# Performance work log

Measured on AMD Instinct MI355X. Metric: run time of the kernel, lower is better.

The kernel has to match this reference:

```python
import jax, jax.numpy as jnp
import numpy as np

BS, NQ, NC = 128, 900, 91
PRE_TOPK = 10000      # source: pre_topk when n_queries*n_cls > 10000
POST_TOPK = 100       # source: keep_inds[:100]
IOU_THRESH = 0.7


def box_cxcywh_to_xyxy(b):
    cx, cy, w, h = b[..., 0], b[..., 1], b[..., 2], b[..., 3]
    return jnp.stack([cx - 0.5 * w, cy - 0.5 * h, cx + 0.5 * w, cy + 0.5 * h], axis=-1)


def nms_image(boxes, scores, labels):
    """Greedy batched NMS, returning the first POST_TOPK picked indices.
    boxes: [PRE,4] xyxy (scaled), scores: [PRE] desc-sorted, labels: [PRE] int.
    batched_nms trick: offset boxes per class so IoU across classes is 0."""
    max_coord = jnp.max(boxes)
    off = labels.astype(boxes.dtype) * (max_coord + 1.0)
    ob = boxes + off[:, None]                          # [PRE,4]
    areas = (ob[:, 2] - ob[:, 0]) * (ob[:, 3] - ob[:, 1])

    def step(active, _):
        s = jnp.where(active, scores, -jnp.inf)
        i = jnp.argmax(s)                              # highest-score surviving box
        bi = ob[i]
        xx1 = jnp.maximum(bi[0], ob[:, 0])
        yy1 = jnp.maximum(bi[1], ob[:, 1])
        xx2 = jnp.minimum(bi[2], ob[:, 2])
        yy2 = jnp.minimum(bi[3], ob[:, 3])
        inter = jnp.clip(xx2 - xx1, 0.0) * jnp.clip(yy2 - yy1, 0.0)
        union = areas[i] + areas - inter
        iou = inter / jnp.maximum(union, 1e-9)
        # suppress IoU > thresh (includes i itself since iou(i,i)=1)
        active = active & (iou <= IOU_THRESH)
        return active, i

    _, keep = jax.lax.scan(step, jnp.ones(ob.shape[0], dtype=bool), None, length=POST_TOPK)
    return keep                                         # [POST]


def setup_inputs() -> dict:
    key = jax.random.key(0)
    k1, k2, k3, k4 = jax.random.split(key, 4)
    pred_logits = jax.random.normal(k1, (BS, NQ, NC), dtype=jnp.float32) * 2.0 - 2.0
    cxcy = jax.random.uniform(k2, (BS, NQ, 2), dtype=jnp.float32)
    wh = jax.random.uniform(k3, (BS, NQ, 2), dtype=jnp.float32, minval=0.02, maxval=0.3)
    pred_boxes = jnp.concatenate([cxcy, wh], axis=-1)   # cxcywh in [0,1]
    target_sizes = jax.random.uniform(k4, (BS, 2), dtype=jnp.float32, minval=480.0, maxval=1333.0)
    return {"pred_logits": pred_logits, "pred_boxes": pred_boxes, "target_sizes": target_sizes}


def reference(pred_logits, pred_boxes, target_sizes):
    bs, nq, nc = pred_logits.shape
    prob = jax.nn.sigmoid(pred_logits).reshape(bs, nq * nc)      # all_scores
    boxes = box_cxcywh_to_xyxy(pred_boxes)                        # [bs,nq,4]
    img_h, img_w = target_sizes[:, 0], target_sizes[:, 1]
    scale = jnp.stack([img_w, img_h, img_w, img_h], axis=1)       # [bs,4]
    boxes = boxes * scale[:, None, :]

    top_scores, top_idx = jax.lax.top_k(prob, PRE_TOPK)           # [bs,PRE]
    top_labels = top_idx % nc                                     # all_labels gather
    top_box_idx = top_idx // nc                                   # all_boxes gather
    top_boxes = jnp.take_along_axis(boxes, top_box_idx[..., None], axis=1)  # [bs,PRE,4]

    keep = jax.vmap(nms_image)(top_boxes, top_scores, top_labels)  # [bs,POST]
    out_scores = jnp.take_along_axis(top_scores, keep, axis=1)
    out_labels = jnp.take_along_axis(top_labels, keep, axis=1)
    out_boxes = jnp.take_along_axis(top_boxes, keep[..., None], axis=1)
    return out_scores, out_labels, out_boxes
```

## Files before the change

### kernel.cpp

```cpp
#include <hip/hip_runtime.h>
#include <cstdint>

#pragma clang fp contract(off)

#define BS   128
#define NQ   900
#define NC   91
#define NQC  (NQ * NC)
#define Q4   (NQC / 4)
#define HHALF 10238
#define PRE  10000
#define POST 100
#define TBITS 13
#define TBINS (1 << TBITS)
#define TSHIFT (32 - TBITS)
#define K_WIN 16
#define HSEG 1024
#define KS   2780
#define CAPH 7680
#define NSLOT 15

typedef unsigned long long ull;

#define WS_CNT 0
#define WS_KEYS 8192

__device__ __forceinline__ uint32_t fkey(float f) {
    uint32_t b = __float_as_uint(f);
    return (b & 0x80000000u) ? ~b : (b | 0x80000000u);
}
__device__ __forceinline__ float unkey(uint32_t u) {
    uint32_t b = (u & 0x80000000u) ? (u & 0x7FFFFFFFu) : ~u;
    return __uint_as_float(b);
}
__device__ __forceinline__ uint32_t qclamp(uint32_t q) { return (q < NQ) ? q : (NQ - 1); }

__device__ __forceinline__ ull shflx(ull v, int j) {
    uint32_t lo = (uint32_t)__shfl_xor((int)(uint32_t)v, j, 64);
    uint32_t hi = (uint32_t)__shfl_xor((int)(uint32_t)(v >> 32), j, 64);
    return ((ull)hi << 32) | (ull)lo;
}
__device__ __forceinline__ ull cex(ull v, int j, bool lower, bool desc) {
    ull pb = shflx(v, j);
    ull a = lower ? v : pb;
    ull b = lower ? pb : v;
    bool sw = desc ? (a < b) : (a > b);
    return sw ? pb : v;
}
__device__ __forceinline__ void ce(ull& a, ull& b, bool desc) {
    bool sw = desc ? (a < b) : (a > b);
    if (sw) { ull t = a; a = b; b = t; }
}

__global__ void __launch_bounds__(1024) k_compact(const float* __restrict__ logits,
                                                  ull* __restrict__ keys,
                                                  uint32_t* __restrict__ cnts) {
    const int img = blockIdx.x >> 1;
    const int h = blockIdx.x & 1;
    const int tid = threadIdx.x;
    const int lane = tid & 63;
    __shared__ uint32_t hist[TBINS];
    __shared__ uint32_t part[1024];
    __shared__ uint32_t sTB, sCnt;
    const float4* lg4 = (const float4*)(logits + (size_t)img * NQC);
    for (int i = tid; i < TBINS; i += 1024) hist[i] = 0u;
    if (tid == 0) sCnt = 0u;
    float4 sv[5];
    #pragma unroll
    for (int c = 0; c < 5; ++c) sv[c] = lg4[c * 4096 + tid];
    __syncthreads();
    #pragma unroll
    for (int c = 0; c < 5; ++c) {
        atomicAdd(&hist[fkey(sv[c].x) >> TSHIFT], 1u);
        atomicAdd(&hist[fkey(sv[c].y) >> TSHIFT], 1u);
        atomicAdd(&hist[fkey(sv[c].z) >> TSHIFT], 1u);
        atomicAdd(&hist[fkey(sv[c].w) >> TSHIFT], 1u);
    }
    __syncthreads();
    {
        uint32_t s = 0;
        int b0 = tid * 8;
        #pragma unroll
        for (int j = 0; j < 8; ++j) s += hist[b0 + j];
        part[tid] = s;
    }
    __syncthreads();
    if (tid < 64) {
        uint32_t pv[16]; uint32_t tot = 0;
        #pragma unroll
        for (int j = 0; j < 16; ++j) { pv[j] = part[tid * 16 + j]; tot += pv[j]; }
        uint32_t sinc = tot;
        #pragma unroll
        for (int off = 1; off < 64; off <<= 1) {
            uint32_t o = (uint32_t)__shfl_down((int)sinc, off, 64);
            if (tid + off < 64) sinc += o;
        }
        uint32_t cum = sinc - tot;
        for (int j = 15; j >= 0; --j) {
            if (cum < KS && cum + pv[j] >= KS) {
                int pbn = (tid * 16 + j) * 8;
                uint32_t c2 = cum;
                for (int b = pbn + 7; b >= pbn; --b) {
                    if (c2 + hist[b] >= KS) { sTB = (uint32_t)b; break; }
                    c2 += hist[b];
                }
            }
            cum += pv[j];
        }
    }
    __syncthreads();
    const uint32_t TB = sTB;
    ull* seg = keys + (size_t)(img * 2 + h) * CAPH;
    const int lo = h * HHALF;
    const int hi = (lo + HHALF < Q4) ? (lo + HHALF) : Q4;
    for (int i0 = lo; i0 < hi; i0 += 1024) {
        int i = i0 + tid;
        bool inb = (i < hi);
        float4 v = inb ? lg4[i] : make_float4(0.f, 0.f, 0.f, 0.f);
        float comp[4] = {v.x, v.y, v.z, v.w};
        #pragma unroll
        for (int c = 0; c < 4; ++c) {
            uint32_t u = fkey(comp[c]);
            bool pass = inb && ((u >> TSHIFT) >= TB);
            ull m = __ballot(pass);
            if (m) {
                uint32_t wb = 0u;
                if (lane == 0) wb = atomicAdd(&sCnt, (uint32_t)__popcll(m));
                wb = (uint32_t)__shfl((int)wb, 0, 64);
                if (pass) {
                    uint32_t p = wb + (uint32_t)__popcll(m & ((1ull << lane) - 1ull));
                    uint32_t fi = (uint32_t)(i * 4 + c);
                    if (p < CAPH) seg[p] = ((ull)u << 32) | (ull)(0xFFFFFFFFu - fi);
                }
            }
        }
    }
    __syncthreads();
    if (tid == 0) cnts[img * 2 + h] = (sCnt < CAPH) ? sCnt : CAPH;
}

__global__ void __launch_bounds__(1024) k_sel(const ull* __restrict__ keys,
                                              const uint32_t* __restrict__ cnts,
                                              const float* __restrict__ pred_boxes,
                                              const float* __restrict__ target_sizes,
                                              float* __restrict__ out) {
    const int img = blockIdx.x;
    const int tid = threadIdx.x;
    const int lane = tid & 63;
    const int wv = tid >> 6;

    __shared__ uint32_t hist[TBINS];
    __shared__ uint32_t part[1024];
    __shared__ float4 shPB[NQ];
    __shared__ ull binK[HSEG];
    __shared__ ull headK[HSEG];
    __shared__ float aX1[POST], aY1[POST], aX2[POST], aY2[POST], aAr[POST];
    __shared__ int   aCl[POST];
    __shared__ float s_x1[K_WIN], s_y1[K_WIN], s_x2[K_WIN], s_y2[K_WIN];
    __shared__ int   s_cl[K_WIN];
    __shared__ uint32_t s_em[K_WIN];
    __shared__ ull sF0;
    __shared__ uint32_t sCntA, sCntB, sMX;
    __shared__ uint32_t sB1, sTp1, sB2, sTp2, sTK;

    const float ih = target_sizes[img * 2 + 0];
    const float iw = target_sizes[img * 2 + 1];
    const float* pb = pred_boxes + (size_t)img * NQ * 4;

    auto mckey = [&](uint32_t f) -> uint32_t {
        uint32_t q = qclamp(f / NC);
        float4 bb = shPB[q];
        float x1 = (bb.x - 0.5f * bb.z) * iw;
        float y1 = (bb.y - 0.5f * bb.w) * ih;
        float x2 = (bb.x + 0.5f * bb.z) * iw;
        float y2 = (bb.y + 0.5f * bb.w) * ih;
        return fkey(fmaxf(fmaxf(x1, y1), fmaxf(x2, y2)));
    };

    if (tid < NQ) shPB[tid] = ((const float4*)pb)[tid];
    for (int i = tid; i < TBINS; i += 1024) hist[i] = 0u;
    binK[tid] = 0ull; headK[tid] = 0ull;
    if (tid == 0) { sCntA = 0u; sCntB = 0u; sMX = 0u; sF0 = 0ull;
                    sB1 = 0u; sTp1 = 1u; sB2 = 0u; sTp2 = 0u; sTK = 0u; }
    const uint32_t c0 = cnts[img * 2 + 0];
    const uint32_t c1 = cnts[img * 2 + 1];
    const int total = (int)(c0 + c1);
    const ull* seg0 = keys + (size_t)(img * 2) * CAPH;
    const ull* seg1 = seg0 + CAPH;
    ull kk[NSLOT];
    #pragma unroll
    for (int j = 0; j < NSLOT; ++j) {
        int i = tid + (j << 10);
        ull x = 0ull;
        if (i < total) x = (i < (int)c0) ? seg0[i] : seg1[i - (int)c0];
        kk[j] = x;
    }
    __syncthreads();

    #pragma unroll
    for (int j = 0; j < NSLOT; ++j) {
        ull x = kk[j];
        if (x != 0ull) atomicAdd(&hist[(uint32_t)(x >> 51)], 1u);
    }
    __syncthreads();
    {
        uint32_t s = 0;
        int b0 = tid * 8;
        #pragma unroll
        for (int j = 0; j < 8; ++j) s += hist[b0 + j];
        part[tid] = s;
    }
    __syncthreads();
    if (tid < 64) {
        uint32_t pv[16]; uint32_t tot = 0;
        #pragma unroll
        for (int j = 0; j < 16; ++j) { pv[j] = part[tid * 16 + j]; tot += pv[j]; }
        uint32_t sinc = tot;
        #pragma unroll
        for (int off = 1; off < 64; off <<= 1) {
            uint32_t o = (uint32_t)__shfl_down((int)sinc, off, 64);
            if (tid + off < 64) sinc += o;
        }
        uint32_t tt = (uint32_t)__shfl((int)sinc, 0, 64);
        uint32_t TKl = (tt < PRE) ? tt : PRE;
        uint32_t T2l = (TKl < HSEG) ? TKl : HSEG;
        if (tid == 0) sTK = TKl;
        uint32_t cum = sinc - tot;
        for (int j = 15; j >= 0; --j) {
            if (cum < TKl && cum + pv[j] >= TKl) {
                int pbn = (tid * 16 + j) * 8;
                uint32_t c2 = cum;
                for (int b = pbn + 7; b >= pbn; --b) {
                    if (c2 + hist[b] >= TKl) { sB1 = (uint32_t)b; sTp1 = TKl - c2; break; }
                    c2 += hist[b];
                }
            }
            if (cum < T2l && cum + pv[j] >= T2l) {
                int pbn = (tid * 16 + j) * 8;
                uint32_t c2 = cum;
                for (int b = pbn + 7; b >= pbn; --b) {
                    if (c2 + hist[b] >= T2l) { sB2 = (uint32_t)b; sTp2 = T2l - c2; break; }
                    c2 += hist[b];
                }
            }
            cum += pv[j];
        }
    }
    __syncthreads();
    const uint32_t B1 = sB1, tp1 = sTp1, B2 = sB2;
    const uint32_t TK = sTK;
    const int C1 = (int)(((TK < (uint32_t)HSEG) ? TK : (uint32_t)HSEG) - sTp2);

    uint32_t lmx = 0u;
    #pragma unroll
    for (int j = 0; j < NSLOT; ++j) {
        ull x = kk[j];
        uint32_t bin = (uint32_t)(x >> 51);
        bool liveK = (x != 0ull);
        if (liveK && bin > B1) { uint32_t km = mckey(~(uint32_t)x); if (km > lmx) lmx = km; }
        bool isA = liveK && (bin == B1);
        bool isB = liveK && (bin > B2);
        ull mA = __ballot(isA);
        if (mA) {
            uint32_t wb = 0u;
            if (lane == 0) wb = atomicAdd(&sCntA, (uint32_t)__popcll(mA));
            wb = (uint32_t)__shfl((int)wb, 0, 64);
            if (isA) {
                uint32_t p = wb + (uint32_t)__popcll(mA & ((1ull << lane) - 1ull));
                if (p < HSEG) binK[p] = x;
            }
        }
        ull mB = __ballot(isB);
        if (mB) {
            uint32_t wb = 0u;
            if (lane == 0) wb = atomicAdd(&sCntB, (uint32_t)__popcll(mB));
            wb = (uint32_t)__shfl((int)wb, 0, 64);
            if (isB) {
                uint32_t p = wb + (uint32_t)__popcll(mB & ((1ull << lane) - 1ull));
                if (p < HSEG) headK[p] = x;
            }
        }
    }
    __syncthreads();

    {
        ull r0 = 0, r1 = 0, r2 = 0, r3 = 0;
        const int cw = wv & 3;
        const int cb = cw << 8;
        ull* A = (wv < 4) ? binK : headK;
        if (wv < 8) {
            r0 = A[cb | lane]; r1 = A[cb | 64 | lane];
            r2 = A[cb | 128 | lane]; r3 = A[cb | 192 | lane];
            #pragma unroll
            for (int k2 = 2; k2 <= 32; k2 <<= 1) {
                bool d = ((lane & k2) == 0);
                #pragma unroll
                for (int j = 16; j >= 1; j >>= 1) {
                    if (j <= (k2 >> 1)) {
                        bool lw = ((lane & j) == 0);
                        r0 = cex(r0, j, lw, d); r1 = cex(r1, j, lw, d);
                        r2 = cex(r2, j, lw, d); r3 = cex(r3, j, lw, d);
                    }
                }
            }
            #pragma unroll
            for (int j = 32; j >= 1; j >>= 1) {
                bool lw = ((lane & j) == 0);
                r0 = cex(r0, j, lw, true);  r1 = cex(r1, j, lw, false);
                r2 = cex(r2, j, lw, true);  r3 = cex(r3, j, lw, false);
            }
            ce(r0, r1, true); ce(r2, r3, false);
            #pragma unroll
            for (int j = 32; j >= 1; j >>= 1) {
                bool lw = ((lane & j) == 0);
                r0 = cex(r0, j, lw, true);  r1 = cex(r1, j, lw, true);
                r2 = cex(r2, j, lw, false); r3 = cex(r3, j, lw, false);
            }
            {
                bool d = ((cw & 1) == 0);
                ce(r0, r2, d); ce(r1, r3, d); ce(r0, r1, d); ce(r2, r3, d);
                #pragma unroll
                for (int j = 32; j >= 1; j >>= 1) {
                    bool lw = ((lane & j) == 0);
                    r0 = cex(r0, j, lw, d); r1 = cex(r1, j, lw, d);
                    r2 = cex(r2, j, lw, d); r3 = cex(r3, j, lw, d);
                }
            }
            A[cb | lane] = r0; A[cb | 64 | lane] = r1;
            A[cb | 128 | lane] = r2; A[cb | 192 | lane] = r3;
        }
        __syncthreads();
        {
            ull* Bp = (tid >> 9) ? headK : binK;
            int t = tid & 511;
            int i = ((t & ~255) << 1) | (t & 255);
            int ixj = i | 256;
            bool d = ((i & 512) == 0);
            ull a = Bp[i], b = Bp[ixj];
            bool sw = d ? (a < b) : (a > b);
            if (sw) { Bp[i] = b; Bp[ixj] = a; }
        }
        __syncthreads();
        if (wv < 8) {
            r0 = A[cb | lane]; r1 = A[cb | 64 | lane];
            r2 = A[cb | 128 | lane]; r3 = A[cb | 192 | lane];
            bool d = ((cw & 2) == 0);
            ce(r0, r2, d); ce(r1, r3, d); ce(r0, r1, d); ce(r2, r3, d);
            #pragma unroll
            for (int j = 32; j >= 1; j >>= 1) {
                bool lw = ((lane & j) == 0);
                r0 = cex(r0, j, lw, d); r1 = cex(r1, j, lw, d);
                r2 = cex(r2, j, lw, d); r3 = cex(r3, j, lw, d);
            }
            A[cb | lane] = r0; A[cb | 64 | lane] = r1;
            A[cb | 128 | lane] = r2; A[cb | 192 | lane] = r3;
        }
        __syncthreads();
        {
            ull* Bp = (tid >> 9) ? headK : binK;
            int t = tid & 511;
            ull a = Bp[t], b = Bp[t | 512];
            if (a < b) { Bp[t] = b; Bp[t | 512] = a; }
        }
        __syncthreads();
        {
            ull* Bp = (tid >> 9) ? headK : binK;
            int t = tid & 511;
            int i = ((t & ~255) << 1) | (t & 255);
            int ixj = i | 256;
            ull a = Bp[i], b = Bp[ixj];
            if (a < b) { Bp[i] = b; Bp[ixj] = a; }
        }
        __syncthreads();
        if (wv < 8) {
            r0 = A[cb | lane]; r1 = A[cb | 64 | lane];
            r2 = A[cb | 128 | lane]; r3 = A[cb | 192 | lane];
            ce(r0, r2, true); ce(r1, r3, true); ce(r0, r1, true); ce(r2, r3, true);
            #pragma unroll
            for (int j = 32; j >= 1; j >>= 1) {
                bool lw = ((lane & j) == 0);
                r0 = cex(r0, j, lw, true); r1 = cex(r1, j, lw, true);
                r2 = cex(r2, j, lw, true); r3 = cex(r3, j, lw, true);
            }
            A[cb | lane] = r0; A[cb | 64 | lane] = r1;
            A[cb | 128 | lane] = r2; A[cb | 192 | lane] = r3;
        }
        __syncthreads();
    }

    if (tid < (int)tp1) {
        ull x = binK[tid];
        if (x != 0ull) { uint32_t km = mckey(~(uint32_t)x); if (km > lmx) lmx = km; }
    }
    for (int off = 32; off > 0; off >>= 1) {
        uint32_t o = (uint32_t)__shfl_down((int)lmx, off, 64);
        if (o > lmx) lmx = o;
    }
    if (lane == 0) atomicMax(&sMX, lmx);
    if (tid == 0 && C1 > 0) sF0 = headK[0];
    __syncthreads();
    float offD;
    {
        uint32_t m = sMX;
        uint32_t b = (m & 0x80000000u) ? (m & 0x7FFFFFFFu) : ~m;
        offD = __uint_as_float(b) + 1.0f;
    }

    auto sort1024 = [&]() {
        const int idx = tid;
        ull x = headK[idx];
        #pragma unroll
        for (int k2 = 2; k2 <= 32; k2 <<= 1) {
            bool d = ((lane & k2) == 0);
            #pragma unroll
            for (int j = 16; j >= 1; j >>= 1)
                if (j <= (k2 >> 1)) x = cex(x, j, (lane & j) == 0, d);
        }
        {
            bool d = ((idx & 64) == 0);
            #pragma unroll
            for (int j = 32; j >= 1; j >>= 1) x = cex(x, j, (lane & j) == 0, d);
        }
        for (int k = 128; k <= 1024; k <<= 1) {
            headK[idx] = x;
            __syncthreads();
            for (int j = k >> 1; j >= 64; j >>= 1) {
                if (tid < 512) {
                    int i2 = ((tid & ~(j - 1)) << 1) | (tid & (j - 1));
                    int ixj = i2 | j;
                    ull a = headK[i2], b = headK[ixj];
                    bool sw = ((i2 & k) == 0) ? (a < b) : (a > b);
                    if (sw) { headK[i2] = b; headK[ixj] = a; }
                }
                __syncthreads();
            }
            x = headK[idx];
            bool d = ((idx & k) == 0);
            #pragma unroll
            for (int j = 32; j >= 1; j >>= 1) x = cex(x, j, (lane & j) == 0, d);
        }
        headK[idx] = x;
        __syncthreads();
    };

    int npick = 0, base = 0, segbase = 0, segend = C1;
    int bcur = (int)B2;
    bool needF0 = (C1 == 0);
    while (npick < POST) {
        if (base >= segend) {
            if (segend >= (int)TK) {
                ull x0 = sF0;
                uint32_t f0 = ~(uint32_t)x0;
                uint32_t u0 = (uint32_t)(x0 >> 32);
                uint32_t q0 = qclamp(f0 / NC);
                uint32_t cc0 = f0 - (f0 / NC) * NC;
                float4 bb = shPB[q0];
                float rx1 = (bb.x - 0.5f * bb.z) * iw;
                float ry1 = (bb.y - 0.5f * bb.w) * ih;
                float rx2 = (bb.x + 0.5f * bb.z) * iw;
                float ry2 = (bb.y + 0.5f * bb.w) * ih;
                float sc = 1.0f / (1.0f + expf(-unkey(u0)));
                for (int p2 = npick + tid; p2 < POST; p2 += 1024) {
                    out[img * POST + p2] = sc;
                    out[BS * POST + img * POST + p2] = (float)cc0;
                    float* ob2 = out + 2 * BS * POST + ((size_t)img * POST + p2) * 4;
                    ob2[0] = rx1; ob2[1] = ry1; ob2[2] = rx2; ob2[3] = ry2;
                }
                break;
            }
            while (bcur > 0 && hist[bcur] == 0u) --bcur;
            headK[tid] = 0ull;
            if (tid == 0) sCntA = 0u;
            __syncthreads();
            for (int i0 = 0; i0 < total; i0 += 1024) {
                int i = i0 + tid;
                ull x = 0ull;
                if (i < total) x = (i < (int)c0) ? seg0[i] : seg1[i - (int)c0];
                bool pass = (x != 0ull) && ((uint32_t)(x >> 51) == (uint32_t)bcur);
                ull m = __ballot(pass);
                if (m) {
                    uint32_t wb = 0u;
                    if (lane == 0) wb = atomicAdd(&sCntA, (uint32_t)__popcll(m));
                    wb = (uint32_t)__shfl((int)wb, 0, 64);
                    if (pass) {
                        uint32_t p = wb + (uint32_t)__popcll(m & ((1ull << lane) - 1ull));
                        if (p < HSEG) headK[p] = x;
                    }
                }
            }
            __syncthreads();
            sort1024();
            int avail = (int)((sCntA < (uint32_t)HSEG) ? sCntA : (uint32_t)HSEG);
            int take = (int)TK - segend; if (take > avail) take = avail;
            if (needF0) { if (tid == 0) sF0 = headK[0]; needF0 = false; __syncthreads(); }
            segbase = segend; segend += take; --bcur;
            continue;
        }

        const int r = base + wv;
        const bool val = (r < segend);
        const ull xk = headK[val ? (r - segbase) : 0];
        const uint32_t f = val ? ~(uint32_t)xk : 0u;
        const uint32_t uk = (uint32_t)(xk >> 32);
        const uint32_t q = qclamp(f / NC);
        const uint32_t cc = f - (f / NC) * NC;
        float4 bb = shPB[q];
        const float x1 = (bb.x - 0.5f * bb.z) * iw;
        const float y1 = (bb.y - 0.5f * bb.w) * ih;
        const float x2 = (bb.x + 0.5f * bb.z) * iw;
        const float y2 = (bb.y + 0.5f * bb.w) * ih;
        if (lane == 0) {
            s_x1[wv] = x1; s_y1[wv] = y1; s_x2[wv] = x2; s_y2[wv] = y2;
            s_cl[wv] = val ? (int)cc : -1;
        }
        __syncthreads();

        const float o = (float)cc * offD;
        const float cx1 = x1 + o, cy1 = y1 + o, cx2 = x2 + o, cy2 = y2 + o;
        const float car = (cx2 - cx1) * (cy2 - cy1);
        bool cf = false;
        if (val && lane < wv && s_cl[lane] == (int)cc) {
            float jx1 = s_x1[lane] + o, jy1 = s_y1[lane] + o;
            float jx2 = s_x2[lane] + o, jy2 = s_y2[lane] + o;
            float arj = (jx2 - jx1) * (jy2 - jy1);
            float xx1 = fmaxf(jx1, cx1), yy1 = fmaxf(jy1, cy1);
            float xx2 = fminf(jx2, cx2), yy2 = fminf(jy2, cy2);
            float inter = fmaxf(xx2 - xx1, 0.0f) * fmaxf(yy2 - yy1, 0.0f);
            float uni = (arj + car) - inter;
            float iou = inter / fmaxf(uni, 1e-9f);
            cf = !(iou <= 0.7f);
        }
        uint32_t em = (uint32_t)(__ballot(cf) & 0xFFFFull);
        bool pf = false;
        for (int i2 = lane; i2 < npick; i2 += 64) {
            if (aCl[i2] == (int)cc) {
                float jx1 = aX1[i2] + o, jy1 = aY1[i2] + o;
                float jx2 = aX2[i2] + o, jy2 = aY2[i2] + o;
                float arj = aAr[i2];
                float xx1 = fmaxf(jx1, cx1), yy1 = fmaxf(jy1, cy1);
                float xx2 = fminf(jx2, cx2), yy2 = fminf(jy2, cy2);
                float inter = fmaxf(xx2 - xx1, 0.0f) * fmaxf(yy2 - yy1, 0.0f);
                float uni = (arj + car) - inter;
                float iou = inter / fmaxf(uni, 1e-9f);
                pf |= !(iou <= 0.7f);
            }
        }
        bool anyPrior = (__ballot(pf) != 0ull);
        if (lane == 0)
            s_em[wv] = em | (anyPrior ? 0x80000000u : 0u) | (val ? 0u : 0x40000000u);
        __syncthreads();

        uint32_t acc = 0u; int a = 0;
        const int room = POST - npick;
        #pragma unroll
        for (int w2 = 0; w2 < K_WIN; ++w2) {
            uint32_t ew = s_em[w2];
            if (!(ew & 0xC0000000u) && a < room && ((ew & 0xFFFFu & acc) == 0u)) {
                acc |= (1u << w2); ++a;
            }
        }

        if (((acc >> wv) & 1u) && lane == 0) {
            int p = npick + __popc(acc & ((1u << wv) - 1u));
            float sc = 1.0f / (1.0f + expf(-unkey(uk)));
            out[img * POST + p] = sc;
            out[BS * POST + img * POST + p] = (float)cc;
            float* ob2 = out + 2 * BS * POST + ((size_t)img * POST + p) * 4;
            ob2[0] = x1; ob2[1] = y1; ob2[2] = x2; ob2[3] = y2;
            aX1[p] = x1; aY1[p] = y1; aX2[p] = x2; aY2[p] = y2;
            aAr[p] = car; aCl[p] = (int)cc;
        }
        npick += a;
        base += K_WIN;
    }
}

extern "C" void kernel_launch(void* const* d_in, const int* in_sizes, int n_in,
                              void* d_out, int out_size, void* d_ws, size_t ws_size,
                              hipStream_t stream) {
    const float* logits = (const float*)d_in[0];
    const float* boxes  = (const float*)d_in[1];
    const float* tsizes = (const float*)d_in[2];
    float* out = (float*)d_out;

    uint32_t* cnts = (uint32_t*)((char*)d_ws + WS_CNT);
    ull* keys = (ull*)((char*)d_ws + WS_KEYS);

    k_compact<<<2 * BS, 1024, 0, stream>>>(logits, keys, cnts);
    k_sel<<<BS, 1024, 0, stream>>>(keys, cnts, boxes, tsizes, out);
}
```

Baseline: 138.8 us.

## Precompute selection histograms in compact kernel and widen NMS window to 64

The compact kernel now builds a histogram of the candidate keys it writes and stores it to global memory as uint16 per half-image. The select kernel sums the two half histograms instead of re-histogramming every candidate with shared atomics. The greedy NMS window grows from 16 to 64 candidates per round, with each wave handling four candidates, so there are fewer block-wide synchronisations. In exchange, each round does more speculative IoU work that may be wasted, and the kernels use more registers and extra workspace.

Measured after the change: 146.9 us. 1.06x slower.

```diff
diff --git a/kernel.cpp b/kernel.cpp
--- a/kernel.cpp
+++ b/kernel.cpp
@@ -14,7 +14,7 @@
 #define TBITS 13
 #define TBINS (1 << TBITS)
 #define TSHIFT (32 - TBITS)
-#define K_WIN 16
+#define K_WIN 64
 #define HSEG 1024
 #define KS   2780
 #define CAPH 7680
@@ -23,7 +23,8 @@
 typedef unsigned long long ull;
 
 #define WS_CNT 0
-#define WS_KEYS 8192
+#define WS_GH  4096
+#define WS_KEYS (4096 + 4*1024*1024)
 
 __device__ __forceinline__ uint32_t fkey(float f) {
     uint32_t b = __float_as_uint(f);
@@ -54,6 +55,7 @@
 
 __global__ void __launch_bounds__(1024) k_compact(const float* __restrict__ logits,
                                                   ull* __restrict__ keys,
+                                                  uint16_t* __restrict__ ghist,
                                                   uint32_t* __restrict__ cnts) {
     const int img = blockIdx.x >> 1;
     const int h = blockIdx.x & 1;
@@ -110,6 +112,8 @@
     }
     __syncthreads();
     const uint32_t TB = sTB;
+    for (int i = tid; i < TBINS; i += 1024) hist[i] = 0u;
+    __syncthreads();
     ull* seg = keys + (size_t)(img * 2 + h) * CAPH;
     const int lo = h * HHALF;
     const int hi = (lo + HHALF < Q4) ? (lo + HHALF) : Q4;
@@ -130,16 +134,22 @@
                 if (pass) {
                     uint32_t p = wb + (uint32_t)__popcll(m & ((1ull << lane) - 1ull));
                     uint32_t fi = (uint32_t)(i * 4 + c);
-                    if (p < CAPH) seg[p] = ((ull)u << 32) | (ull)(0xFFFFFFFFu - fi);
-                }
-            }
-        }
-    }
-    __syncthreads();
+                    if (p < CAPH) {
+                        seg[p] = ((ull)u << 32) | (ull)(0xFFFFFFFFu - fi);
+                        atomicAdd(&hist[u >> TSHIFT], 1u);
+                    }
+                }
+            }
+        }
+    }
+    __syncthreads();
+    uint16_t* g = ghist + (size_t)(img * 2 + h) * TBINS;
+    for (int i = tid; i < TBINS; i += 1024) g[i] = (uint16_t)hist[i];
     if (tid == 0) cnts[img * 2 + h] = (sCnt < CAPH) ? sCnt : CAPH;
 }
 
 __global__ void __launch_bounds__(1024) k_sel(const ull* __restrict__ keys,
+                                              const uint16_t* __restrict__ ghist,
                                               const uint32_t* __restrict__ cnts,
                                               const float* __restrict__ pred_boxes,
                                               const float* __restrict__ target_sizes,
@@ -158,7 +168,7 @@
     __shared__ int   aCl[POST];
     __shared__ float s_x1[K_WIN], s_y1[K_WIN], s_x2[K_WIN], s_y2[K_WIN];
     __shared__ int   s_cl[K_WIN];
-    __shared__ uint32_t s_em[K_WIN];
+    __shared__ ull   s_em[K_WIN];
     __shared__ ull sF0;
     __shared__ uint32_t sCntA, sCntB, sMX;
     __shared__ uint32_t sB1, sTp1, sB2, sTp2, sTK;
@@ -178,10 +188,22 @@
     };
 
     if (tid < NQ) shPB[tid] = ((const float4*)pb)[tid];
-    for (int i = tid; i < TBINS; i += 1024) hist[i] = 0u;
     binK[tid] = 0ull; headK[tid] = 0ull;
     if (tid == 0) { sCntA = 0u; sCntB = 0u; sMX = 0u; sF0 = 0ull;
                     sB1 = 0u; sTp1 = 1u; sB2 = 0u; sTp2 = 0u; sTK = 0u; }
+    {
+        const uint16_t* g0 = ghist + (size_t)(img * 2) * TBINS;
+        const uint16_t* g1 = g0 + TBINS;
+        uint32_t s = 0;
+        int b0 = tid * 8;
+        #pragma unroll
+        for (int j = 0; j < 8; ++j) {
+            uint32_t hv = (uint32_t)g0[b0 + j] + (uint32_t)g1[b0 + j];
+            hist[b0 + j] = hv;
+            s += hv;
+        }
+        part[tid] = s;
+    }
     const uint32_t c0 = cnts[img * 2 + 0];
     const uint32_t c1 = cnts[img * 2 + 1];
     const int total = (int)(c0 + c1);
@@ -197,20 +219,6 @@
     }
     __syncthreads();
 
-    #pragma unroll
-    for (int j = 0; j < NSLOT; ++j) {
-        ull x = kk[j];
-        if (x != 0ull) atomicAdd(&hist[(uint32_t)(x >> 51)], 1u);
-    }
-    __syncthreads();
-    {
-        uint32_t s = 0;
-        int b0 = tid * 8;
-        #pragma unroll
-        for (int j = 0; j < 8; ++j) s += hist[b0 + j];
-        part[tid] = s;
-    }
-    __syncthreads();
     if (tid < 64) {
         uint32_t pv[16]; uint32_t tot = 0;
         #pragma unroll
@@ -497,78 +505,111 @@
             continue;
         }
 
-        const int r = base + wv;
-        const bool val = (r < segend);
-        const ull xk = headK[val ? (r - segbase) : 0];
-        const uint32_t f = val ? ~(uint32_t)xk : 0u;
-        const uint32_t uk = (uint32_t)(xk >> 32);
-        const uint32_t q = qclamp(f / NC);
-        const uint32_t cc = f - (f / NC) * NC;
-        float4 bb = shPB[q];
-        const float x1 = (bb.x - 0.5f * bb.z) * iw;
-        const float y1 = (bb.y - 0.5f * bb.w) * ih;
-        const float x2 = (bb.x + 0.5f * bb.z) * iw;
-        const float y2 = (bb.y + 0.5f * bb.w) * ih;
+        bool valv[4]; uint32_t ccv[4], ukv[4];
+        float X1[4], Y1[4], X2[4], Y2[4];
+        #pragma unroll
+        for (int off = 0; off < 4; ++off) {
+            const int ci = 4 * wv + off;
+            const int r = base + ci;
+            valv[off] = (r < segend);
+            const ull xk = headK[valv[off] ? (r - segbase) : 0];
+            const uint32_t f = valv[off] ? ~(uint32_t)xk : 0u;
+            ukv[off] = (uint32_t)(xk >> 32);
+            const uint32_t q = qclamp(f / NC);
+            ccv[off] = f - (f / NC) * NC;
+            float4 bb = shPB[q];
+            X1[off] = (bb.x - 0.5f * bb.z) * iw;
+            Y1[off] = (bb.y - 0.5f * bb.w) * ih;
+            X2[off] = (bb.x + 0.5f * bb.z) * iw;
+            Y2[off] = (bb.y + 0.5f * bb.w) * ih;
+        }
         if (lane == 0) {
-            s_x1[wv] = x1; s_y1[wv] = y1; s_x2[wv] = x2; s_y2[wv] = y2;
-            s_cl[wv] = val ? (int)cc : -1;
-        }
-        __syncthreads();
-
-        const float o = (float)cc * offD;
-        const float cx1 = x1 + o, cy1 = y1 + o, cx2 = x2 + o, cy2 = y2 + o;
-        const float car = (cx2 - cx1) * (cy2 - cy1);
-        bool cf = false;
-        if (val && lane < wv && s_cl[lane] == (int)cc) {
-            float jx1 = s_x1[lane] + o, jy1 = s_y1[lane] + o;
-            float jx2 = s_x2[lane] + o, jy2 = s_y2[lane] + o;
-            float arj = (jx2 - jx1) * (jy2 - jy1);
-            float xx1 = fmaxf(jx1, cx1), yy1 = fmaxf(jy1, cy1);
-            float xx2 = fminf(jx2, cx2), yy2 = fminf(jy2, cy2);
-            float inter = fmaxf(xx2 - xx1, 0.0f) * fmaxf(yy2 - yy1, 0.0f);
-            float uni = (arj + car) - inter;
-            float iou = inter / fmaxf(uni, 1e-9f);
-            cf = !(iou <= 0.7f);
-        }
-        uint32_t em = (uint32_t)(__ballot(cf) & 0xFFFFull);
-        bool pf = false;
+            #pragma unroll
+            for (int off = 0; off < 4; ++off) {
+                const int ci = 4 * wv + off;
+                s_x1[ci] = X1[off]; s_y1[ci] = Y1[off];
+                s_x2[ci] = X2[off]; s_y2[ci] = Y2[off];
+                s_cl[ci] = valv[off] ? (int)ccv[off] : -1;
+            }
+        }
+        __syncthreads();
+
+        float ov[4], CX1[4], CY1[4], CX2[4], CY2[4], CAR[4];
+        ull emv[4];
+        #pragma unroll
+        for (int off = 0; off < 4; ++off) {
+            const int ci = 4 * wv + off;
+            const float o = (float)ccv[off] * offD;
+            ov[off] = o;
+            CX1[off] = X1[off] + o; CY1[off] = Y1[off] + o;
+            CX2[off] = X2[off] + o; CY2[off] = Y2[off] + o;
+            CAR[off] = (CX2[off] - CX1[off]) * (CY2[off] - CY1[off]);
+            bool cf = false;
+            if (valv[off] && lane < ci && s_cl[lane] == (int)ccv[off]) {
+                float jx1 = s_x1[lane] + o, jy1 = s_y1[lane] + o;
+                float jx2 = s_x2[lane] + o, jy2 = s_y2[lane] + o;
+                float arj = (jx2 - jx1) * (jy2 - jy1);
+                float xx1 = fmaxf(jx1, CX1[off]), yy1 = fmaxf(jy1, CY1[off]);
+                float xx2 = fminf(jx2, CX2[off]), yy2 = fminf(jy2, CY2[off]);
+                float inter = fmaxf(xx2 - xx1, 0.0f) * fmaxf(yy2 - yy1, 0.0f);
+                float uni = (arj + CAR[off]) - inter;
+                float iou = inter / fmaxf(uni, 1e-9f);
+                cf = !(iou <= 0.7f);
+            }
+            emv[off] = __ballot(cf) & ((ci == 0) ? 0ull : ((ci >= 64) ? ~0ull : ((1ull << ci) - 1ull)));
+        }
+        bool pf[4] = {false, false, false, false};
         for (int i2 = lane; i2 < npick; i2 += 64) {
-            if (aCl[i2] == (int)cc) {
-                float jx1 = aX1[i2] + o, jy1 = aY1[i2] + o;
-                float jx2 = aX2[i2] + o, jy2 = aY2[i2] + o;
-                float arj = aAr[i2];
-                float xx1 = fmaxf(jx1, cx1), yy1 = fmaxf(jy1, cy1);
-                float xx2 = fminf(jx2, cx2), yy2 = fminf(jy2, cy2);
-                float inter = fmaxf(xx2 - xx1, 0.0f) * fmaxf(yy2 - yy1, 0.0f);
-                float uni = (arj + car) - inter;
-                float iou = inter / fmaxf(uni, 1e-9f);
-                pf |= !(iou <= 0.7f);
-            }
-        }
-        bool anyPrior = (__ballot(pf) != 0ull);
-        if (lane == 0)
-            s_em[wv] = em | (anyPrior ? 0x80000000u : 0u) | (val ? 0u : 0x40000000u);
-        __syncthreads();
-
-        uint32_t acc = 0u; int a = 0;
+            const int acl = aCl[i2];
+            const float ax1 = aX1[i2], ay1 = aY1[i2], ax2 = aX2[i2], ay2 = aY2[i2];
+            const float aar = aAr[i2];
+            #pragma unroll
+            for (int off = 0; off < 4; ++off) {
+                if (valv[off] && acl == (int)ccv[off]) {
+                    float jx1 = ax1 + ov[off], jy1 = ay1 + ov[off];
+                    float jx2 = ax2 + ov[off], jy2 = ay2 + ov[off];
+                    float xx1 = fmaxf(jx1, CX1[off]), yy1 = fmaxf(jy1, CY1[off]);
+                    float xx2 = fminf(jx2, CX2[off]), yy2 = fminf(jy2, CY2[off]);
+                    float inter = fmaxf(xx2 - xx1, 0.0f) * fmaxf(yy2 - yy1, 0.0f);
+                    float uni = (aar + CAR[off]) - inter;
+                    float iou = inter / fmaxf(uni, 1e-9f);
+                    pf[off] |= !(iou <= 0.7f);
+                }
+            }
+        }
+        #pragma unroll
+        for (int off = 0; off < 4; ++off) {
+            bool anyP = (__ballot(pf[off]) != 0ull);
+            if (lane == 0) {
+                const int ci = 4 * wv + off;
+                s_em[ci] = emv[off] | ((anyP || !valv[off]) ? (1ull << 63) : 0ull);
+            }
+        }
+        __syncthreads();
+
+        ull acc = 0ull; int a = 0;
         const int room = POST - npick;
         #pragma unroll
-        for (int w2 = 0; w2 < K_WIN; ++w2) {
-            uint32_t ew = s_em[w2];
-            if (!(ew & 0xC0000000u) && a < room && ((ew & 0xFFFFu & acc) == 0u)) {
-                acc |= (1u << w2); ++a;
-            }
-        }
-
-        if (((acc >> wv) & 1u) && lane == 0) {
-            int p = npick + __popc(acc & ((1u << wv) - 1u));
-            float sc = 1.0f / (1.0f + expf(-unkey(uk)));
-            out[img * POST + p] = sc;
-            out[BS * POST + img * POST + p] = (float)cc;
-            float* ob2 = out + 2 * BS * POST + ((size_t)img * POST + p) * 4;
-            ob2[0] = x1; ob2[1] = y1; ob2[2] = x2; ob2[3] = y2;
-            aX1[p] = x1; aY1[p] = y1; aX2[p] = x2; aY2[p] = y2;
-            aAr[p] = car; aCl[p] = (int)cc;
+        for (int ci = 0; ci < K_WIN; ++ci) {
+            ull ew = s_em[ci];
+            if (!(ew >> 63) && a < room && ((ew & acc) == 0ull)) {
+                acc |= (1ull << ci); ++a;
+            }
+        }
+
+        #pragma unroll
+        for (int off = 0; off < 4; ++off) {
+            const int ci = 4 * wv + off;
+            if (((acc >> ci) & 1ull) && lane == off) {
+                int p = npick + (int)__popcll(acc & ((1ull << ci) - 1ull));
+                float sc = 1.0f / (1.0f + expf(-unkey(ukv[off])));
+                out[img * POST + p] = sc;
+                out[BS * POST + img * POST + p] = (float)ccv[off];
+                float* ob2 = out + 2 * BS * POST + ((size_t)img * POST + p) * 4;
+                ob2[0] = X1[off]; ob2[1] = Y1[off]; ob2[2] = X2[off]; ob2[3] = Y2[off];
+                aX1[p] = X1[off]; aY1[p] = Y1[off]; aX2[p] = X2[off]; aY2[p] = Y2[off];
+                aAr[p] = CAR[off]; aCl[p] = (int)ccv[off];
+            }
         }
         npick += a;
         base += K_WIN;
@@ -584,8 +625,9 @@
     float* out = (float*)d_out;
 
     uint32_t* cnts = (uint32_t*)((char*)d_ws + WS_CNT);
+    uint16_t* ghist = (uint16_t*)((char*)d_ws + WS_GH);
     ull* keys = (ull*)((char*)d_ws + WS_KEYS);
 
-    k_compact<<<2 * BS, 1024, 0, stream>>>(logits, keys, cnts);
-    k_sel<<<BS, 1024, 0, stream>>>(keys, cnts, boxes, tsizes, out);
-}
+    k_compact<<<2 * BS, 1024, 0, stream>>>(logits, keys, ghist, cnts);
+    k_sel<<<BS, 1024, 0, stream>>>(keys, ghist, cnts, boxes, tsizes, out);
+}
```

## Build selection histogram during compaction and batch per-wave atomics in compact loop

Applied to the files above, without the earlier changes.

The compaction kernel now builds a 13-bit histogram of the kept keys while writing them and stores it to workspace as uint16. The selection kernel reads both half-histograms instead of rebuilding one with shared atomics over all loaded keys, which removes a histogram pass and two barriers there. The compact loop also handles two float4 per thread per iteration and makes one atomic reservation per wave for all eight components instead of one per component. In exchange, compaction does extra shared atomics and global histogram writes, and the workspace layout grows.

Result: no change. 138.2 us (-0.4%).

```diff
diff --git a/kernel.cpp b/kernel.cpp
--- a/kernel.cpp
+++ b/kernel.cpp
@@ -23,7 +23,8 @@
 typedef unsigned long long ull;
 
 #define WS_CNT 0
-#define WS_KEYS 8192
+#define WS_GH  4096
+#define WS_KEYS (4096 + 4*1024*1024)
 
 __device__ __forceinline__ uint32_t fkey(float f) {
     uint32_t b = __float_as_uint(f);
@@ -54,6 +55,7 @@
 
 __global__ void __launch_bounds__(1024) k_compact(const float* __restrict__ logits,
                                                   ull* __restrict__ keys,
+                                                  uint16_t* __restrict__ ghist,
                                                   uint32_t* __restrict__ cnts) {
     const int img = blockIdx.x >> 1;
     const int h = blockIdx.x & 1;
@@ -110,36 +112,61 @@
     }
     __syncthreads();
     const uint32_t TB = sTB;
+    for (int i = tid; i < TBINS; i += 1024) hist[i] = 0u;
+    __syncthreads();
     ull* seg = keys + (size_t)(img * 2 + h) * CAPH;
     const int lo = h * HHALF;
     const int hi = (lo + HHALF < Q4) ? (lo + HHALF) : Q4;
-    for (int i0 = lo; i0 < hi; i0 += 1024) {
-        int i = i0 + tid;
-        bool inb = (i < hi);
-        float4 v = inb ? lg4[i] : make_float4(0.f, 0.f, 0.f, 0.f);
-        float comp[4] = {v.x, v.y, v.z, v.w};
-        #pragma unroll
-        for (int c = 0; c < 4; ++c) {
-            uint32_t u = fkey(comp[c]);
-            bool pass = inb && ((u >> TSHIFT) >= TB);
-            ull m = __ballot(pass);
-            if (m) {
-                uint32_t wb = 0u;
-                if (lane == 0) wb = atomicAdd(&sCnt, (uint32_t)__popcll(m));
-                wb = (uint32_t)__shfl((int)wb, 0, 64);
-                if (pass) {
-                    uint32_t p = wb + (uint32_t)__popcll(m & ((1ull << lane) - 1ull));
-                    uint32_t fi = (uint32_t)(i * 4 + c);
-                    if (p < CAPH) seg[p] = ((ull)u << 32) | (ull)(0xFFFFFFFFu - fi);
-                }
-            }
-        }
-    }
-    __syncthreads();
+    for (int i0 = lo; i0 < hi; i0 += 2048) {
+        float4 v[2]; bool inb[2]; int ii[2];
+        #pragma unroll
+        for (int s = 0; s < 2; ++s) {
+            int i = i0 + (s << 10) + tid;
+            ii[s] = i; inb[s] = (i < hi);
+            v[s] = inb[s] ? lg4[i] : make_float4(0.f, 0.f, 0.f, 0.f);
+        }
+        uint32_t u[8]; bool pass[8];
+        #pragma unroll
+        for (int s = 0; s < 2; ++s) {
+            u[s * 4 + 0] = fkey(v[s].x); u[s * 4 + 1] = fkey(v[s].y);
+            u[s * 4 + 2] = fkey(v[s].z); u[s * 4 + 3] = fkey(v[s].w);
+            #pragma unroll
+            for (int c = 0; c < 4; ++c)
+                pass[s * 4 + c] = inb[s] && ((u[s * 4 + c] >> TSHIFT) >= TB);
+        }
+        ull m[8]; uint32_t pc[8]; uint32_t tot = 0;
+        #pragma unroll
+        for (int c = 0; c < 8; ++c) {
+            m[c] = __ballot(pass[c]);
+            pc[c] = (uint32_t)__popcll(m[c]);
+            tot += pc[c];
+        }
+        uint32_t wb = 0u;
+        if (lane == 0 && tot) wb = atomicAdd(&sCnt, tot);
+        wb = (uint32_t)__shfl((int)wb, 0, 64);
+        ull lm = (1ull << lane) - 1ull;
+        uint32_t off = 0;
+        #pragma unroll
+        for (int c = 0; c < 8; ++c) {
+            if (pass[c]) {
+                uint32_t p = wb + off + (uint32_t)__popcll(m[c] & lm);
+                uint32_t fi = (uint32_t)(ii[c >> 2] * 4 + (c & 3));
+                if (p < CAPH) {
+                    seg[p] = ((ull)u[c] << 32) | (ull)(0xFFFFFFFFu - fi);
+                    atomicAdd(&hist[u[c] >> TSHIFT], 1u);
+                }
+            }
+            off += pc[c];
+        }
+    }
+    __syncthreads();
+    uint16_t* g = ghist + (size_t)(img * 2 + h) * TBINS;
+    for (int i = tid; i < TBINS; i += 1024) g[i] = (uint16_t)hist[i];
     if (tid == 0) cnts[img * 2 + h] = (sCnt < CAPH) ? sCnt : CAPH;
 }
 
 __global__ void __launch_bounds__(1024) k_sel(const ull* __restrict__ keys,
+                                              const uint16_t* __restrict__ ghist,
                                               const uint32_t* __restrict__ cnts,
                                               const float* __restrict__ pred_boxes,
                                               const float* __restrict__ target_sizes,
@@ -178,10 +205,22 @@
     };
 
     if (tid < NQ) shPB[tid] = ((const float4*)pb)[tid];
-    for (int i = tid; i < TBINS; i += 1024) hist[i] = 0u;
     binK[tid] = 0ull; headK[tid] = 0ull;
     if (tid == 0) { sCntA = 0u; sCntB = 0u; sMX = 0u; sF0 = 0ull;
                     sB1 = 0u; sTp1 = 1u; sB2 = 0u; sTp2 = 0u; sTK = 0u; }
+    {
+        const uint16_t* g0 = ghist + (size_t)(img * 2) * TBINS;
+        const uint16_t* g1 = g0 + TBINS;
+        uint32_t s = 0;
+        int b0 = tid * 8;
+        #pragma unroll
+        for (int j = 0; j < 8; ++j) {
+            uint32_t hv = (uint32_t)g0[b0 + j] + (uint32_t)g1[b0 + j];
+            hist[b0 + j] = hv;
+            s += hv;
+        }
+        part[tid] = s;
+    }
     const uint32_t c0 = cnts[img * 2 + 0];
     const uint32_t c1 = cnts[img * 2 + 1];
     const int total = (int)(c0 + c1);
@@ -197,20 +236,6 @@
     }
     __syncthreads();
 
-    #pragma unroll
-    for (int j = 0; j < NSLOT; ++j) {
-        ull x = kk[j];
-        if (x != 0ull) atomicAdd(&hist[(uint32_t)(x >> 51)], 1u);
-    }
-    __syncthreads();
-    {
-        uint32_t s = 0;
-        int b0 = tid * 8;
-        #pragma unroll
-        for (int j = 0; j < 8; ++j) s += hist[b0 + j];
-        part[tid] = s;
-    }
-    __syncthreads();
     if (tid < 64) {
         uint32_t pv[16]; uint32_t tot = 0;
         #pragma unroll
@@ -584,8 +609,9 @@
     float* out = (float*)d_out;
 
     uint32_t* cnts = (uint32_t*)((char*)d_ws + WS_CNT);
+    uint16_t* ghist = (uint16_t*)((char*)d_ws + WS_GH);
     ull* keys = (ull*)((char*)d_ws + WS_KEYS);
 
-    k_compact<<<2 * BS, 1024, 0, stream>>>(logits, keys, cnts);
-    k_sel<<<BS, 1024, 0, stream>>>(keys, cnts, boxes, tsizes, out);
-}
+    k_compact<<<2 * BS, 1024, 0, stream>>>(logits, keys, ghist, cnts);
+    k_sel<<<BS, 1024, 0, stream>>>(keys, ghist, cnts, boxes, tsizes, out);
+}
```
